# Kernel optimization log

Hardware: AMD Instinct MI355X
Metric: run time of the kernel (lower is better)

## Reference

```python
import jax, jax.numpy as jnp
import numpy as np

BS, GRID, LSTM_H, CNN_C, PROJ = 256, 49, 512, 2048, 512


def setup_inputs() -> dict:
    key = jax.random.key(0)
    ks = jax.random.split(key, 7)
    s = lambda fan_in: 1.0 / np.sqrt(fan_in)
    return {
        "lstm_hidden": jax.random.normal(ks[0], (BS, LSTM_H), jnp.float32),
        "cnn_feat": jax.random.normal(ks[1], (BS, GRID, CNN_C), jnp.float32),
        "W_lstm": jax.random.normal(ks[2], (PROJ, LSTM_H), jnp.float32) * s(LSTM_H),
        "b_lstm": jax.random.normal(ks[3], (PROJ,), jnp.float32) * s(LSTM_H),
        "W_cnn": jax.random.normal(ks[4], (PROJ, CNN_C), jnp.float32) * s(CNN_C),
        "b_cnn": jax.random.normal(ks[5], (PROJ,), jnp.float32) * s(CNN_C),
        "w_attn": jax.random.normal(ks[6], (1, PROJ), jnp.float32) * s(PROJ),
    }


def reference(lstm_hidden, cnn_feat, W_lstm, b_lstm, W_cnn, b_cnn, w_attn):
    # H computed once (original loop recomputes it per grid, identically)
    H = lstm_hidden @ W_lstm.T + b_lstm                       # (bs, P)
    V = jnp.einsum("bgc,pc->bgp", cnn_feat, W_cnn) + b_cnn    # (bs, G, P)
    z = jnp.tanh(H[:, None, :] + V) @ w_attn[0]               # (bs, G)
    bs, G = z.shape
    # Faithful to torch: cat over grids along dim 0 -> (G*bs,), then view(bs, G)
    z_scrambled = jnp.swapaxes(z, 0, 1).reshape(bs, G)
    return jax.nn.softmax(z_scrambled, axis=1)
```

## Files before the change

kernel.cpp:

```cpp
#include <hip/hip_runtime.h>
#include <math.h>

#define BSZ    256
#define GRID_N 49
#define LSTMH  512
#define CNN_C  2048
#define PROJ   512
#define KAUG   2560
#define M_TOT  12544
#define BK     64
#define KTILES (KAUG / BK)

#define MT     64
#define NT     128
#define NBLK   ((M_TOT / MT) * (PROJ / NT))

#define MT2    128
#define NT2    128
#define NBLK2  ((M_TOT / MT2) * (PROJ / NT2))

#define ACHUNKS (M_TOT * CNN_C / 8)
#define LCHUNKS (BSZ * LSTMH / 8)
#define ABLK    ((ACHUNKS + LCHUNKS) / 256)
#define WBLK    640
#define PBLK    (ABLK + WBLK)

typedef short bf16x8 __attribute__((ext_vector_type(8)));
typedef float f32x4  __attribute__((ext_vector_type(4)));

static __device__ __forceinline__ unsigned short bf16_rne(float f) {
    unsigned int u = __float_as_uint(f);
    u = u + 0x7FFFu + ((u >> 16) & 1u);
    return (unsigned short)(u >> 16);
}
static __device__ __forceinline__ uint4 pack8f(const float* f) {
    uint4 o;
    o.x = (unsigned int)bf16_rne(f[0]) | ((unsigned int)bf16_rne(f[1]) << 16);
    o.y = (unsigned int)bf16_rne(f[2]) | ((unsigned int)bf16_rne(f[3]) << 16);
    o.z = (unsigned int)bf16_rne(f[4]) | ((unsigned int)bf16_rne(f[5]) << 16);
    o.w = (unsigned int)bf16_rne(f[6]) | ((unsigned int)bf16_rne(f[7]) << 16);
    return o;
}
static __device__ __forceinline__ float tanh_fast(float x) {
    float e = __expf(2.f * x);
    return 1.f - 2.f / (e + 1.f);
}
static __device__ __forceinline__ void glds16(const void* g, void* l) {
    __builtin_amdgcn_global_load_lds(
        (const __attribute__((address_space(1))) unsigned int*)g,
        (__attribute__((address_space(3))) unsigned int*)l, 16, 0, 0);
}

__global__ __launch_bounds__(256) void prep_all(
    const float* __restrict__ cnn, const float* __restrict__ lstm,
    const float* __restrict__ Wc,  const float* __restrict__ Wl,
    unsigned short* __restrict__ wsW, unsigned short* __restrict__ wsA,
    unsigned short* __restrict__ wsL, float* __restrict__ out)
{
    const int bid = blockIdx.x, t = threadIdx.x;
    if (bid < 49) out[bid * 256 + t] = 0.f;
    float f[8];
    if (bid < ABLK) {
        const int c = bid * 256 + t;
        const float* src; unsigned short* dst;
        if (c < ACHUNKS) { src = cnn  + (size_t)c * 8; dst = wsA + (size_t)c * 8; }
        else { const int c2 = c - ACHUNKS; src = lstm + (size_t)c2 * 8; dst = wsL + (size_t)c2 * 8; }
        *(float4*)&f[0] = ((const float4*)src)[0];
        *(float4*)&f[4] = ((const float4*)src)[1];
        *(uint4*)dst = pack8f(f);
    } else {
        const int c  = (bid - ABLK) * 256 + t;
        const int p  = c / 320;
        const int kc = (c % 320) * 8;
        const float* src = (kc < CNN_C) ? (Wc + (size_t)p * CNN_C + kc)
                                        : (Wl + (size_t)p * LSTMH + (kc - CNN_C));
        *(float4*)&f[0] = ((const float4*)src)[0];
        *(float4*)&f[4] = ((const float4*)src)[1];
        *(uint4*)(wsW + (size_t)p * KAUG + kc) = pack8f(f);
    }
}

__global__ __launch_bounds__(256, 2) void gemm2(
    const unsigned short* __restrict__ wsW, const unsigned short* __restrict__ wsA,
    const unsigned short* __restrict__ wsL,
    const float* __restrict__ bl, const float* __restrict__ bc,
    const float* __restrict__ wat, float* __restrict__ out)
{
    __shared__ unsigned short Ab[2][MT2][BK];
    __shared__ unsigned short Bb[2][NT2][BK];

    const int t   = threadIdx.x;
    const int w   = t >> 6;
    const int l   = t & 63;
    const int q   = l >> 4;
    const int r16 = l & 15;
    const int wr  = w >> 1;
    const int wc  = w & 1;

    const int bid = (int)blockIdx.x;
    const int swz = (bid & 7) * (NBLK2 / 8) + (bid >> 3);
    const int m0  = (swz >> 2) * MT2;
    const int n0  = (swz & 3) * NT2;

    const int srow = l >> 3;
    const int cg   = (l & 7) ^ srow;

    auto stage = [&](int kt, int bufi) {
        const int k0 = kt * BK;
        #pragma unroll
        for (int jj = 0; jj < 4; ++jj) {
            const int rowb = w * 32 + jj * 8;
            const unsigned short* g = wsW + (size_t)(n0 + rowb + srow) * KAUG + k0 + cg * 8;
            glds16(g, &Bb[bufi][rowb][0]);
        }
        if (k0 < CNN_C) {
            #pragma unroll
            for (int jj = 0; jj < 4; ++jj) {
                const int rowa = w * 32 + jj * 8;
                const unsigned short* g = wsA + (size_t)(m0 + rowa + srow) * CNN_C + k0 + cg * 8;
                glds16(g, &Ab[bufi][rowa][0]);
            }
        } else {
            const int k0l = k0 - CNN_C;
            #pragma unroll
            for (int jj = 0; jj < 4; ++jj) {
                const int rowa = w * 32 + jj * 8;
                const int rg   = m0 + rowa + srow;
                const unsigned short* g = wsL + (size_t)(rg / 49) * LSTMH + k0l + cg * 8;
                glds16(g, &Ab[bufi][rowa][0]);
            }
        }
    };

    f32x4 acc[4][4];
    #pragma unroll
    for (int mt = 0; mt < 4; ++mt)
        #pragma unroll
        for (int nt = 0; nt < 4; ++nt)
            acc[mt][nt] = (f32x4){0.f, 0.f, 0.f, 0.f};

    stage(0, 0);
    asm volatile("s_waitcnt vmcnt(0)" ::: "memory");
    __builtin_amdgcn_s_barrier();

    int cur = 0;
    for (int kt = 0; kt < KTILES; ++kt) {
        if (kt + 1 < KTILES) stage(kt + 1, cur ^ 1);
        #pragma unroll
        for (int ks = 0; ks < 2; ++ks) {
            const int cp = ((ks * 4 + q) ^ (r16 & 7)) * 8;
            bf16x8 af[4], bfr[4];
            #pragma unroll
            for (int mt = 0; mt < 4; ++mt)
                af[mt] = *(const bf16x8*)&Ab[cur][wr * 64 + mt * 16 + r16][cp];
            #pragma unroll
            for (int nt = 0; nt < 4; ++nt)
                bfr[nt] = *(const bf16x8*)&Bb[cur][wc * 64 + nt * 16 + r16][cp];
            #pragma unroll
            for (int mt = 0; mt < 4; ++mt)
                #pragma unroll
                for (int nt = 0; nt < 4; ++nt)
                    acc[mt][nt] = __builtin_amdgcn_mfma_f32_16x16x32_bf16(
                        af[mt], bfr[nt], acc[mt][nt], 0, 0, 0);
        }
        asm volatile("s_waitcnt vmcnt(0)" ::: "memory");
        __builtin_amdgcn_s_barrier();
        cur ^= 1;
    }

    float* zpf = (float*)&Ab[0][0][0];
    float part[4][4];
    #pragma unroll
    for (int mt = 0; mt < 4; ++mt)
        #pragma unroll
        for (int rr = 0; rr < 4; ++rr) part[mt][rr] = 0.f;
    #pragma unroll
    for (int nt = 0; nt < 4; ++nt) {
        const int p = n0 + wc * 64 + nt * 16 + r16;
        const float bb = bl[p] + bc[p];
        const float wa = wat[p];
        #pragma unroll
        for (int mt = 0; mt < 4; ++mt)
            #pragma unroll
            for (int rr = 0; rr < 4; ++rr)
                part[mt][rr] += tanh_fast(acc[mt][nt][rr] + bb) * wa;
    }
    #pragma unroll
    for (int mt = 0; mt < 4; ++mt)
        #pragma unroll
        for (int rr = 0; rr < 4; ++rr) {
            float v = part[mt][rr];
            v += __shfl_xor(v, 1);
            v += __shfl_xor(v, 2);
            v += __shfl_xor(v, 4);
            v += __shfl_xor(v, 8);
            if (r16 == 0) zpf[wc * MT2 + wr * 64 + mt * 16 + q * 4 + rr] = v;
        }
    __syncthreads();
    if (t < MT2) {
        const float v = zpf[t] + zpf[MT2 + t];
        const int row = m0 + t;
        const int b2  = row / 49;
        const int g2  = row - b2 * 49;
        atomicAdd(&out[g2 * BSZ + b2], v);
    }
}

__global__ __launch_bounds__(256) void prep_w(const float* __restrict__ Wc,
                                              const float* __restrict__ Wl,
                                              unsigned short* __restrict__ wsW) {
    int c  = blockIdx.x * 256 + threadIdx.x;
    int p  = c / 320;
    int kc = (c % 320) * 8;
    const float* src = (kc < CNN_C) ? (Wc + (size_t)p * CNN_C + kc)
                                    : (Wl + (size_t)p * LSTMH + (kc - CNN_C));
    float f[8];
    *(float4*)&f[0] = ((const float4*)src)[0];
    *(float4*)&f[4] = ((const float4*)src)[1];
    *(uint4*)(wsW + (size_t)p * KAUG + kc) = pack8f(f);
}

template <bool WS>
__global__ __launch_bounds__(256, 4) void gemm_k(
    const float* __restrict__ lstm, const float* __restrict__ cnn,
    const float* __restrict__ Wc,   const float* __restrict__ Wl,
    const float* __restrict__ bl,   const float* __restrict__ bc,
    const float* __restrict__ wat,  const unsigned short* __restrict__ wsW,
    float* __restrict__ out)
{
    __shared__ unsigned short Ash[MT][BK];
    __shared__ unsigned short Bsh[NT][BK];
    __shared__ float zp[4][MT];

    const int t   = threadIdx.x;
    const int w   = t >> 6;
    const int l   = t & 63;
    const int q   = l >> 4;
    const int r16 = l & 15;

    const int bid = (int)blockIdx.x;
    const int swz = (bid & 7) * (NBLK / 8) + (bid >> 3);
    const int m0 = (swz >> 2) * MT;
    const int n0 = (swz & 3) * NT;

    const int ra  = t >> 2;
    const int ca0 = t & 3;
    const int sa  = ra & 7;
    const int grow = m0 + ra;
    const int ab   = grow / 49;
    const int ag   = grow - ab * 49;
    const float* cnnb  = cnn + ((size_t)ab * GRID_N + ag) * CNN_C;
    const float* lstmb = lstm + (size_t)ab * LSTMH;

    f32x4 acc[4][2];
    #pragma unroll
    for (int mt = 0; mt < 4; ++mt)
        #pragma unroll
        for (int nt = 0; nt < 2; ++nt)
            acc[mt][nt] = (f32x4){0.f, 0.f, 0.f, 0.f};

    float4 fa0, fa1, fa2, fa3;

    auto a_load = [&](int k0) {
        const float* s = (k0 < CNN_C) ? (cnnb + k0) : (lstmb + (k0 - CNN_C));
        const float4* p0 = (const float4*)(s + ca0 * 8);
        const float4* p1 = (const float4*)(s + (ca0 + 4) * 8);
        fa0 = p0[0]; fa1 = p0[1];
        fa2 = p1[0]; fa3 = p1[1];
    };
    auto a_write = [&]() {
        float f[8];
        *(float4*)&f[0] = fa0; *(float4*)&f[4] = fa1;
        *(uint4*)&Ash[ra][(ca0 ^ sa) * 8] = pack8f(f);
        *(float4*)&f[0] = fa2; *(float4*)&f[4] = fa3;
        *(uint4*)&Ash[ra][((ca0 + 4) ^ sa) * 8] = pack8f(f);
    };
    auto b_stage = [&](int k0) {
        if constexpr (WS) {
            const int rsub = l >> 3;
            const int cg   = (l & 7) ^ rsub;
            #pragma unroll
            for (int j = 0; j < 4; ++j) {
                const int rowb = w * 32 + j * 8;
                const unsigned short* g =
                    wsW + (size_t)(n0 + rowb + rsub) * KAUG + k0 + cg * 8;
                glds16(g, &Bsh[rowb][0]);
            }
        } else {
            const int rb = t >> 1;
            const int hb = t & 1;
            const float* s = (k0 < CNN_C) ? (Wc + (size_t)(n0 + rb) * CNN_C + k0)
                                          : (Wl + (size_t)(n0 + rb) * LSTMH + (k0 - CNN_C));
            const int sw = rb & 7;
            #pragma unroll
            for (int c = 0; c < 4; ++c) {
                const int cc = hb * 4 + c;
                float f[8];
                *(float4*)&f[0] = ((const float4*)(s + cc * 8))[0];
                *(float4*)&f[4] = ((const float4*)(s + cc * 8))[1];
                *(uint4*)&Bsh[rb][(cc ^ sw) * 8] = pack8f(f);
            }
        }
    };

    a_load(0);
    a_write();
    b_stage(0);

    for (int kt = 0; kt < KTILES; ++kt) {
        __syncthreads();
        const bool more = (kt + 1 < KTILES);
        if (more) a_load((kt + 1) * BK);
        #pragma unroll
        for (int ks = 0; ks < 2; ++ks) {
            const int cp = ((ks * 4 + q) ^ (r16 & 7)) * 8;
            bf16x8 af[4], bfr[2];
            #pragma unroll
            for (int mt = 0; mt < 4; ++mt)
                af[mt] = *(const bf16x8*)&Ash[mt * 16 + r16][cp];
            #pragma unroll
            for (int nt = 0; nt < 2; ++nt)
                bfr[nt] = *(const bf16x8*)&Bsh[w * 32 + nt * 16 + r16][cp];
            #pragma unroll
            for (int mt = 0; mt < 4; ++mt)
                #pragma unroll
                for (int nt = 0; nt < 2; ++nt)
                    acc[mt][nt] = __builtin_amdgcn_mfma_f32_16x16x32_bf16(
                        af[mt], bfr[nt], acc[mt][nt], 0, 0, 0);
        }
        __syncthreads();
        if (more) { a_write(); b_stage((kt + 1) * BK); }
    }

    float part[4][4];
    #pragma unroll
    for (int mt = 0; mt < 4; ++mt)
        #pragma unroll
        for (int rr = 0; rr < 4; ++rr) part[mt][rr] = 0.f;
    #pragma unroll
    for (int nt = 0; nt < 2; ++nt) {
        const int p = n0 + w * 32 + nt * 16 + r16;
        const float bb = bl[p] + bc[p];
        const float wa = wat[p];
        #pragma unroll
        for (int mt = 0; mt < 4; ++mt)
            #pragma unroll
            for (int rr = 0; rr < 4; ++rr)
                part[mt][rr] += tanh_fast(acc[mt][nt][rr] + bb) * wa;
    }
    #pragma unroll
    for (int mt = 0; mt < 4; ++mt)
        #pragma unroll
        for (int rr = 0; rr < 4; ++rr) {
            float v = part[mt][rr];
            v += __shfl_xor(v, 1);
            v += __shfl_xor(v, 2);
            v += __shfl_xor(v, 4);
            v += __shfl_xor(v, 8);
            if (r16 == 0) zp[w][mt * 16 + q * 4 + rr] = v;
        }
    __syncthreads();
    if (t < MT) {
        const float v = zp[0][t] + zp[1][t] + zp[2][t] + zp[3][t];
        const int row = m0 + t;
        const int b2  = row / 49;
        const int g2  = row - b2 * 49;
        atomicAdd(&out[g2 * BSZ + b2], v);
    }
}

__global__ __launch_bounds__(64) void softmax_rows(float* __restrict__ out)
{
    const int i = blockIdx.x;
    const int j = threadIdx.x;
    float x = (j < GRID_N) ? out[i * GRID_N + j] : -1e30f;
    float m = x;
    #pragma unroll
    for (int off = 32; off > 0; off >>= 1) m = fmaxf(m, __shfl_xor(m, off));
    float e = (j < GRID_N) ? __expf(x - m) : 0.f;
    float s = e;
    #pragma unroll
    for (int off = 32; off > 0; off >>= 1) s += __shfl_xor(s, off);
    if (j < GRID_N) out[i * GRID_N + j] = e / s;
}

extern "C" void kernel_launch(void* const* d_in, const int* in_sizes, int n_in,
                              void* d_out, int out_size, void* d_ws, size_t ws_size,
                              hipStream_t stream)
{
    const float* lstm = (const float*)d_in[0];
    const float* cnn  = (const float*)d_in[1];
    const float* Wl   = (const float*)d_in[2];
    const float* bl   = (const float*)d_in[3];
    const float* Wc   = (const float*)d_in[4];
    const float* bc   = (const float*)d_in[5];
    const float* wat  = (const float*)d_in[6];
    float* out = (float*)d_out;

    const size_t szW = (size_t)PROJ * KAUG * sizeof(unsigned short);
    const size_t szA = (size_t)M_TOT * CNN_C * sizeof(unsigned short);
    const size_t szL = (size_t)BSZ * LSTMH * sizeof(unsigned short);

    if (ws_size >= szW + szA + szL) {
        unsigned short* wsW = (unsigned short*)d_ws;
        unsigned short* wsA = wsW + (size_t)PROJ * KAUG;
        unsigned short* wsL = wsA + (size_t)M_TOT * CNN_C;
        prep_all<<<dim3(PBLK), dim3(256), 0, stream>>>(cnn, lstm, Wc, Wl, wsW, wsA, wsL, out);
        gemm2<<<dim3(NBLK2), dim3(256), 0, stream>>>(wsW, wsA, wsL, bl, bc, wat, out);
    } else if (ws_size >= szW) {
        hipMemsetAsync(out, 0, (size_t)out_size * sizeof(float), stream);
        unsigned short* wsW = (unsigned short*)d_ws;
        prep_w<<<dim3(WBLK), dim3(256), 0, stream>>>(Wc, Wl, wsW);
        gemm_k<true><<<dim3(NBLK), dim3(256), 0, stream>>>(lstm, cnn, Wc, Wl, bl, bc, wat, wsW, out);
    } else {
        hipMemsetAsync(out, 0, (size_t)out_size * sizeof(float), stream);
        gemm_k<false><<<dim3(NBLK), dim3(256), 0, stream>>>(lstm, cnn, Wc, Wl, bl, bc, wat, nullptr, out);
    }
    softmax_rows<<<dim3(BSZ), dim3(64), 0, stream>>>(out);
}
```

Measured before the change: 218.0 us.

## Fuse fp32-to-bf16 activation conversion into the GEMM mainloop, dropping the prep pass

Drops the separate pass that converted the full cnn_feat and lstm_hidden tensors to bf16 in workspace. The new GEMM loads fp32 activations straight from global memory into registers, packs them to bf16 and writes them into double-buffered LDS while the MFMAs on the current tile run. Only the weight matrix is still pre-converted, and the output zeroing moves into that small kernel. This removes a full-size write and re-read of the activation tensor. In exchange each A tile is read as fp32, twice the bytes, by every N-block, and register pressure in the mainloop goes up.

```diff
diff --git a/kernel.cpp b/kernel.cpp
--- a/kernel.cpp
+++ b/kernel.cpp
@@ -11,19 +11,15 @@
 #define BK     64
 #define KTILES (KAUG / BK)
 
+#define MT2    128
+#define NT2    128
+#define NBLK2  ((M_TOT / MT2) * (PROJ / NT2))
+
 #define MT     64
 #define NT     128
 #define NBLK   ((M_TOT / MT) * (PROJ / NT))
 
-#define MT2    128
-#define NT2    128
-#define NBLK2  ((M_TOT / MT2) * (PROJ / NT2))
-
-#define ACHUNKS (M_TOT * CNN_C / 8)
-#define LCHUNKS (BSZ * LSTMH / 8)
-#define ABLK    ((ACHUNKS + LCHUNKS) / 256)
-#define WBLK    640
-#define PBLK    (ABLK + WBLK)
+#define WBLK   640
 
 typedef short bf16x8 __attribute__((ext_vector_type(8)));
 typedef float f32x4  __attribute__((ext_vector_type(4)));
@@ -51,165 +47,13 @@
         (__attribute__((address_space(3))) unsigned int*)l, 16, 0, 0);
 }
 
-__global__ __launch_bounds__(256) void prep_all(
-    const float* __restrict__ cnn, const float* __restrict__ lstm,
-    const float* __restrict__ Wc,  const float* __restrict__ Wl,
-    unsigned short* __restrict__ wsW, unsigned short* __restrict__ wsA,
-    unsigned short* __restrict__ wsL, float* __restrict__ out)
-{
+__global__ __launch_bounds__(256) void prep_w(const float* __restrict__ Wc,
+                                              const float* __restrict__ Wl,
+                                              unsigned short* __restrict__ wsW,
+                                              float* __restrict__ out) {
     const int bid = blockIdx.x, t = threadIdx.x;
     if (bid < 49) out[bid * 256 + t] = 0.f;
-    float f[8];
-    if (bid < ABLK) {
-        const int c = bid * 256 + t;
-        const float* src; unsigned short* dst;
-        if (c < ACHUNKS) { src = cnn  + (size_t)c * 8; dst = wsA + (size_t)c * 8; }
-        else { const int c2 = c - ACHUNKS; src = lstm + (size_t)c2 * 8; dst = wsL + (size_t)c2 * 8; }
-        *(float4*)&f[0] = ((const float4*)src)[0];
-        *(float4*)&f[4] = ((const float4*)src)[1];
-        *(uint4*)dst = pack8f(f);
-    } else {
-        const int c  = (bid - ABLK) * 256 + t;
-        const int p  = c / 320;
-        const int kc = (c % 320) * 8;
-        const float* src = (kc < CNN_C) ? (Wc + (size_t)p * CNN_C + kc)
-                                        : (Wl + (size_t)p * LSTMH + (kc - CNN_C));
-        *(float4*)&f[0] = ((const float4*)src)[0];
-        *(float4*)&f[4] = ((const float4*)src)[1];
-        *(uint4*)(wsW + (size_t)p * KAUG + kc) = pack8f(f);
-    }
-}
-
-__global__ __launch_bounds__(256, 2) void gemm2(
-    const unsigned short* __restrict__ wsW, const unsigned short* __restrict__ wsA,
-    const unsigned short* __restrict__ wsL,
-    const float* __restrict__ bl, const float* __restrict__ bc,
-    const float* __restrict__ wat, float* __restrict__ out)
-{
-    __shared__ unsigned short Ab[2][MT2][BK];
-    __shared__ unsigned short Bb[2][NT2][BK];
-
-    const int t   = threadIdx.x;
-    const int w   = t >> 6;
-    const int l   = t & 63;
-    const int q   = l >> 4;
-    const int r16 = l & 15;
-    const int wr  = w >> 1;
-    const int wc  = w & 1;
-
-    const int bid = (int)blockIdx.x;
-    const int swz = (bid & 7) * (NBLK2 / 8) + (bid >> 3);
-    const int m0  = (swz >> 2) * MT2;
-    const int n0  = (swz & 3) * NT2;
-
-    const int srow = l >> 3;
-    const int cg   = (l & 7) ^ srow;
-
-    auto stage = [&](int kt, int bufi) {
-        const int k0 = kt * BK;
-        #pragma unroll
-        for (int jj = 0; jj < 4; ++jj) {
-            const int rowb = w * 32 + jj * 8;
-            const unsigned short* g = wsW + (size_t)(n0 + rowb + srow) * KAUG + k0 + cg * 8;
-            glds16(g, &Bb[bufi][rowb][0]);
-        }
-        if (k0 < CNN_C) {
-            #pragma unroll
-            for (int jj = 0; jj < 4; ++jj) {
-                const int rowa = w * 32 + jj * 8;
-                const unsigned short* g = wsA + (size_t)(m0 + rowa + srow) * CNN_C + k0 + cg * 8;
-                glds16(g, &Ab[bufi][rowa][0]);
-            }
-        } else {
-            const int k0l = k0 - CNN_C;
-            #pragma unroll
-            for (int jj = 0; jj < 4; ++jj) {
-                const int rowa = w * 32 + jj * 8;
-                const int rg   = m0 + rowa + srow;
-                const unsigned short* g = wsL + (size_t)(rg / 49) * LSTMH + k0l + cg * 8;
-                glds16(g, &Ab[bufi][rowa][0]);
-            }
-        }
-    };
-
-    f32x4 acc[4][4];
-    #pragma unroll
-    for (int mt = 0; mt < 4; ++mt)
-        #pragma unroll
-        for (int nt = 0; nt < 4; ++nt)
-            acc[mt][nt] = (f32x4){0.f, 0.f, 0.f, 0.f};
-
-    stage(0, 0);
-    asm volatile("s_waitcnt vmcnt(0)" ::: "memory");
-    __builtin_amdgcn_s_barrier();
-
-    int cur = 0;
-    for (int kt = 0; kt < KTILES; ++kt) {
-        if (kt + 1 < KTILES) stage(kt + 1, cur ^ 1);
-        #pragma unroll
-        for (int ks = 0; ks < 2; ++ks) {
-            const int cp = ((ks * 4 + q) ^ (r16 & 7)) * 8;
-            bf16x8 af[4], bfr[4];
-            #pragma unroll
-            for (int mt = 0; mt < 4; ++mt)
-                af[mt] = *(const bf16x8*)&Ab[cur][wr * 64 + mt * 16 + r16][cp];
-            #pragma unroll
-            for (int nt = 0; nt < 4; ++nt)
-                bfr[nt] = *(const bf16x8*)&Bb[cur][wc * 64 + nt * 16 + r16][cp];
-            #pragma unroll
-            for (int mt = 0; mt < 4; ++mt)
-                #pragma unroll
-                for (int nt = 0; nt < 4; ++nt)
-                    acc[mt][nt] = __builtin_amdgcn_mfma_f32_16x16x32_bf16(
-                        af[mt], bfr[nt], acc[mt][nt], 0, 0, 0);
-        }
-        asm volatile("s_waitcnt vmcnt(0)" ::: "memory");
-        __builtin_amdgcn_s_barrier();
-        cur ^= 1;
-    }
-
-    float* zpf = (float*)&Ab[0][0][0];
-    float part[4][4];
-    #pragma unroll
-    for (int mt = 0; mt < 4; ++mt)
-        #pragma unroll
-        for (int rr = 0; rr < 4; ++rr) part[mt][rr] = 0.f;
-    #pragma unroll
-    for (int nt = 0; nt < 4; ++nt) {
-        const int p = n0 + wc * 64 + nt * 16 + r16;
-        const float bb = bl[p] + bc[p];
-        const float wa = wat[p];
-        #pragma unroll
-        for (int mt = 0; mt < 4; ++mt)
-            #pragma unroll
-            for (int rr = 0; rr < 4; ++rr)
-                part[mt][rr] += tanh_fast(acc[mt][nt][rr] + bb) * wa;
-    }
-    #pragma unroll
-    for (int mt = 0; mt < 4; ++mt)
-        #pragma unroll
-        for (int rr = 0; rr < 4; ++rr) {
-            float v = part[mt][rr];
-            v += __shfl_xor(v, 1);
-            v += __shfl_xor(v, 2);
-            v += __shfl_xor(v, 4);
-            v += __shfl_xor(v, 8);
-            if (r16 == 0) zpf[wc * MT2 + wr * 64 + mt * 16 + q * 4 + rr] = v;
-        }
-    __syncthreads();
-    if (t < MT2) {
-        const float v = zpf[t] + zpf[MT2 + t];
-        const int row = m0 + t;
-        const int b2  = row / 49;
-        const int g2  = row - b2 * 49;
-        atomicAdd(&out[g2 * BSZ + b2], v);
-    }
-}
-
-__global__ __launch_bounds__(256) void prep_w(const float* __restrict__ Wc,
-                                              const float* __restrict__ Wl,
-                                              unsigned short* __restrict__ wsW) {
-    int c  = blockIdx.x * 256 + threadIdx.x;
+    int c  = bid * 256 + t;
     int p  = c / 320;
     int kc = (c % 320) * 8;
     const float* src = (kc < CNN_C) ? (Wc + (size_t)p * CNN_C + kc)
@@ -220,13 +64,150 @@
     *(uint4*)(wsW + (size_t)p * KAUG + kc) = pack8f(f);
 }
 
-template <bool WS>
+__global__ __launch_bounds__(256, 2) void gemm3(
+    const float* __restrict__ lstm, const float* __restrict__ cnn,
+    const unsigned short* __restrict__ wsW,
+    const float* __restrict__ bl, const float* __restrict__ bc,
+    const float* __restrict__ wat, float* __restrict__ out)
+{
+    __shared__ unsigned short Ab[2][MT2][BK];
+    __shared__ unsigned short Bb[2][NT2][BK];
+
+    const int t   = threadIdx.x;
+    const int w   = t >> 6;
+    const int l   = t & 63;
+    const int q   = l >> 4;
+    const int r16 = l & 15;
+    const int wr  = w >> 1;
+    const int wc  = w & 1;
+
+    const int bid = (int)blockIdx.x;
+    const int swz = (bid & 7) * (NBLK2 / 8) + (bid >> 3);
+    const int m0  = (swz >> 2) * MT2;
+    const int n0  = (swz & 3) * NT2;
+
+    const int ar  = t >> 1;
+    const int ac0 = (t & 1) * 4;
+    const int sw  = ar & 7;
+    const int grow = m0 + ar;
+    const int ab_  = grow / 49;
+    const int ag_  = grow - ab_ * 49;
+    const float* cnnb  = cnn + ((size_t)ab_ * GRID_N + ag_) * CNN_C;
+    const float* lstmb = lstm + (size_t)ab_ * LSTMH;
+
+    const int srow = l >> 3;
+    const int cg   = (l & 7) ^ srow;
+
+    float4 fa[8];
+    auto a_load = [&](int k0) {
+        const float* s = (((k0 < CNN_C) ? (cnnb + k0) : (lstmb + (k0 - CNN_C)))) + ac0 * 8;
+        #pragma unroll
+        for (int i = 0; i < 8; ++i) fa[i] = ((const float4*)s)[i];
+    };
+    auto a_write = [&](int bufi) {
+        #pragma unroll
+        for (int c = 0; c < 4; ++c) {
+            float f[8];
+            *(float4*)&f[0] = fa[2 * c];
+            *(float4*)&f[4] = fa[2 * c + 1];
+            *(uint4*)&Ab[bufi][ar][((ac0 + c) ^ sw) * 8] = pack8f(f);
+        }
+    };
+    auto b_stage = [&](int k0, int bufi) {
+        #pragma unroll
+        for (int jj = 0; jj < 4; ++jj) {
+            const int rowb = w * 32 + jj * 8;
+            const unsigned short* g = wsW + (size_t)(n0 + rowb + srow) * KAUG + k0 + cg * 8;
+            glds16(g, &Bb[bufi][rowb][0]);
+        }
+    };
+
+    f32x4 acc[4][4];
+    #pragma unroll
+    for (int mt = 0; mt < 4; ++mt)
+        #pragma unroll
+        for (int nt = 0; nt < 4; ++nt)
+            acc[mt][nt] = (f32x4){0.f, 0.f, 0.f, 0.f};
+
+    a_load(0);
+    a_write(0);
+    b_stage(0, 0);
+    asm volatile("s_waitcnt vmcnt(0) lgkmcnt(0)" ::: "memory");
+    __builtin_amdgcn_s_barrier();
+
+    int cur = 0;
+    for (int kt = 0; kt < KTILES; ++kt) {
+        const bool more = (kt + 1 < KTILES);
+        if (more) {
+            a_load((kt + 1) * BK);
+            b_stage((kt + 1) * BK, cur ^ 1);
+        }
+        #pragma unroll
+        for (int ks = 0; ks < 2; ++ks) {
+            const int cp = ((ks * 4 + q) ^ (r16 & 7)) * 8;
+            bf16x8 af[4], bfr[4];
+            #pragma unroll
+            for (int mt = 0; mt < 4; ++mt)
+                af[mt] = *(const bf16x8*)&Ab[cur][wr * 64 + mt * 16 + r16][cp];
+            #pragma unroll
+            for (int nt = 0; nt < 4; ++nt)
+                bfr[nt] = *(const bf16x8*)&Bb[cur][wc * 64 + nt * 16 + r16][cp];
+            #pragma unroll
+            for (int mt = 0; mt < 4; ++mt)
+                #pragma unroll
+                for (int nt = 0; nt < 4; ++nt)
+                    acc[mt][nt] = __builtin_amdgcn_mfma_f32_16x16x32_bf16(
+                        af[mt], bfr[nt], acc[mt][nt], 0, 0, 0);
+        }
+        if (more) a_write(cur ^ 1);
+        asm volatile("s_waitcnt vmcnt(0) lgkmcnt(0)" ::: "memory");
+        __builtin_amdgcn_s_barrier();
+        cur ^= 1;
+    }
+
+    float* zpf = (float*)&Ab[0][0][0];
+    float part[4][4];
+    #pragma unroll
+    for (int mt = 0; mt < 4; ++mt)
+        #pragma unroll
+        for (int rr = 0; rr < 4; ++rr) part[mt][rr] = 0.f;
+    #pragma unroll
+    for (int nt = 0; nt < 4; ++nt) {
+        const int p = n0 + wc * 64 + nt * 16 + r16;
+        const float bb = bl[p] + bc[p];
+        const float wa = wat[p];
+        #pragma unroll
+        for (int mt = 0; mt < 4; ++mt)
+            #pragma unroll
+            for (int rr = 0; rr < 4; ++rr)
+                part[mt][rr] += tanh_fast(acc[mt][nt][rr] + bb) * wa;
+    }
+    #pragma unroll
+    for (int mt = 0; mt < 4; ++mt)
+        #pragma unroll
+        for (int rr = 0; rr < 4; ++rr) {
+            float v = part[mt][rr];
+            v += __shfl_xor(v, 1);
+            v += __shfl_xor(v, 2);
+            v += __shfl_xor(v, 4);
+            v += __shfl_xor(v, 8);
+            if (r16 == 0) zpf[wc * MT2 + wr * 64 + mt * 16 + q * 4 + rr] = v;
+        }
+    __syncthreads();
+    if (t < MT2) {
+        const float v = zpf[t] + zpf[MT2 + t];
+        const int row = m0 + t;
+        const int b2  = row / 49;
+        const int g2  = row - b2 * 49;
+        atomicAdd(&out[g2 * BSZ + b2], v);
+    }
+}
+
 __global__ __launch_bounds__(256, 4) void gemm_k(
     const float* __restrict__ lstm, const float* __restrict__ cnn,
     const float* __restrict__ Wc,   const float* __restrict__ Wl,
     const float* __restrict__ bl,   const float* __restrict__ bc,
-    const float* __restrict__ wat,  const unsigned short* __restrict__ wsW,
-    float* __restrict__ out)
+    const float* __restrict__ wat,  float* __restrict__ out)
 {
     __shared__ unsigned short Ash[MT][BK];
     __shared__ unsigned short Bsh[NT][BK];
@@ -276,30 +257,18 @@
         *(uint4*)&Ash[ra][((ca0 + 4) ^ sa) * 8] = pack8f(f);
     };
     auto b_stage = [&](int k0) {
-        if constexpr (WS) {
-            const int rsub = l >> 3;
-            const int cg   = (l & 7) ^ rsub;
-            #pragma unroll
-            for (int j = 0; j < 4; ++j) {
-                const int rowb = w * 32 + j * 8;
-                const unsigned short* g =
-                    wsW + (size_t)(n0 + rowb + rsub) * KAUG + k0 + cg * 8;
-                glds16(g, &Bsh[rowb][0]);
-            }
-        } else {
-            const int rb = t >> 1;
-            const int hb = t & 1;
-            const float* s = (k0 < CNN_C) ? (Wc + (size_t)(n0 + rb) * CNN_C + k0)
-                                          : (Wl + (size_t)(n0 + rb) * LSTMH + (k0 - CNN_C));
-            const int sw = rb & 7;
-            #pragma unroll
-            for (int c = 0; c < 4; ++c) {
-                const int cc = hb * 4 + c;
-                float f[8];
-                *(float4*)&f[0] = ((const float4*)(s + cc * 8))[0];
-                *(float4*)&f[4] = ((const float4*)(s + cc * 8))[1];
-                *(uint4*)&Bsh[rb][(cc ^ sw) * 8] = pack8f(f);
-            }
+        const int rb = t >> 1;
+        const int hb = t & 1;
+        const float* s = (k0 < CNN_C) ? (Wc + (size_t)(n0 + rb) * CNN_C + k0)
+                                      : (Wl + (size_t)(n0 + rb) * LSTMH + (k0 - CNN_C));
+        const int sw = rb & 7;
+        #pragma unroll
+        for (int c = 0; c < 4; ++c) {
+            const int cc = hb * 4 + c;
+            float f[8];
+            *(float4*)&f[0] = ((const float4*)(s + cc * 8))[0];
+            *(float4*)&f[4] = ((const float4*)(s + cc * 8))[1];
+            *(uint4*)&Bsh[rb][(cc ^ sw) * 8] = pack8f(f);
         }
     };
 
@@ -398,23 +367,14 @@
     float* out = (float*)d_out;
 
     const size_t szW = (size_t)PROJ * KAUG * sizeof(unsigned short);
-    const size_t szA = (size_t)M_TOT * CNN_C * sizeof(unsigned short);
-    const size_t szL = (size_t)BSZ * LSTMH * sizeof(unsigned short);
-
-    if (ws_size >= szW + szA + szL) {
+
+    if (ws_size >= szW) {
         unsigned short* wsW = (unsigned short*)d_ws;
-        unsigned short* wsA = wsW + (size_t)PROJ * KAUG;
-        unsigned short* wsL = wsA + (size_t)M_TOT * CNN_C;
-        prep_all<<<dim3(PBLK), dim3(256), 0, stream>>>(cnn, lstm, Wc, Wl, wsW, wsA, wsL, out);
-        gemm2<<<dim3(NBLK2), dim3(256), 0, stream>>>(wsW, wsA, wsL, bl, bc, wat, out);
-    } else if (ws_size >= szW) {
-        hipMemsetAsync(out, 0, (size_t)out_size * sizeof(float), stream);
-        unsigned short* wsW = (unsigned short*)d_ws;
-        prep_w<<<dim3(WBLK), dim3(256), 0, stream>>>(Wc, Wl, wsW);
-        gemm_k<true><<<dim3(NBLK), dim3(256), 0, stream>>>(lstm, cnn, Wc, Wl, bl, bc, wat, wsW, out);
+        prep_w<<<dim3(WBLK), dim3(256), 0, stream>>>(Wc, Wl, wsW, out);
+        gemm3<<<dim3(NBLK2), dim3(256), 0, stream>>>(lstm, cnn, wsW, bl, bc, wat, out);
     } else {
         hipMemsetAsync(out, 0, (size_t)out_size * sizeof(float), stream);
-        gemm_k<false><<<dim3(NBLK), dim3(256), 0, stream>>>(lstm, cnn, Wc, Wl, bl, bc, wat, nullptr, out);
+        gemm_k<<<dim3(NBLK), dim3(256), 0, stream>>>(lstm, cnn, Wc, Wl, bl, bc, wat, out);
     }
     softmax_rows<<<dim3(BSZ), dim3(64), 0, stream>>>(out);
 }
```

Result: slower. 265.0 us (+21.6%).

## Split GEMM tile across eight waves with raised MFMA priority

Applied to the files above, without the earlier changes.

The main GEMM kernel now runs 512 threads (8 waves in a 2x4 grid) on the same 128x128 output tile, so each wave holds half the accumulators and the block asks for higher occupancy. It also raises wave priority around the MFMA section and waits on LDS counters before the barrier. The epilogue reduction now sums four column-wave partials. The intermediate workspace fallback path is removed. The risk is more barrier and synchronisation overhead and lower per-wave data reuse in exchange for more latency hiding.

```diff
diff --git a/kernel.cpp b/kernel.cpp
--- a/kernel.cpp
+++ b/kernel.cpp
@@ -11,13 +11,13 @@
 #define BK     64
 #define KTILES (KAUG / BK)
 
+#define MT2    128
+#define NT2    128
+#define NBLK2  ((M_TOT / MT2) * (PROJ / NT2))
+
 #define MT     64
 #define NT     128
 #define NBLK   ((M_TOT / MT) * (PROJ / NT))
-
-#define MT2    128
-#define NT2    128
-#define NBLK2  ((M_TOT / MT2) * (PROJ / NT2))
 
 #define ACHUNKS (M_TOT * CNN_C / 8)
 #define LCHUNKS (BSZ * LSTMH / 8)
@@ -80,7 +80,7 @@
     }
 }
 
-__global__ __launch_bounds__(256, 2) void gemm2(
+__global__ __launch_bounds__(512, 4) void gemm4(
     const unsigned short* __restrict__ wsW, const unsigned short* __restrict__ wsA,
     const unsigned short* __restrict__ wsL,
     const float* __restrict__ bl, const float* __restrict__ bc,
@@ -94,8 +94,8 @@
     const int l   = t & 63;
     const int q   = l >> 4;
     const int r16 = l & 15;
-    const int wr  = w >> 1;
-    const int wc  = w & 1;
+    const int wr  = w >> 2;
+    const int wc  = w & 3;
 
     const int bid = (int)blockIdx.x;
     const int swz = (bid & 7) * (NBLK2 / 8) + (bid >> 3);
@@ -108,23 +108,23 @@
     auto stage = [&](int kt, int bufi) {
         const int k0 = kt * BK;
         #pragma unroll
-        for (int jj = 0; jj < 4; ++jj) {
-            const int rowb = w * 32 + jj * 8;
+        for (int j = 0; j < 2; ++j) {
+            const int rowb = w * 16 + j * 8;
             const unsigned short* g = wsW + (size_t)(n0 + rowb + srow) * KAUG + k0 + cg * 8;
             glds16(g, &Bb[bufi][rowb][0]);
         }
         if (k0 < CNN_C) {
             #pragma unroll
-            for (int jj = 0; jj < 4; ++jj) {
-                const int rowa = w * 32 + jj * 8;
+            for (int j = 0; j < 2; ++j) {
+                const int rowa = w * 16 + j * 8;
                 const unsigned short* g = wsA + (size_t)(m0 + rowa + srow) * CNN_C + k0 + cg * 8;
                 glds16(g, &Ab[bufi][rowa][0]);
             }
         } else {
             const int k0l = k0 - CNN_C;
             #pragma unroll
-            for (int jj = 0; jj < 4; ++jj) {
-                const int rowa = w * 32 + jj * 8;
+            for (int j = 0; j < 2; ++j) {
+                const int rowa = w * 16 + j * 8;
                 const int rg   = m0 + rowa + srow;
                 const unsigned short* g = wsL + (size_t)(rg / 49) * LSTMH + k0l + cg * 8;
                 glds16(g, &Ab[bufi][rowa][0]);
@@ -132,11 +132,11 @@
         }
     };
 
-    f32x4 acc[4][4];
-    #pragma unroll
-    for (int mt = 0; mt < 4; ++mt)
-        #pragma unroll
-        for (int nt = 0; nt < 4; ++nt)
+    f32x4 acc[4][2];
+    #pragma unroll
+    for (int mt = 0; mt < 4; ++mt)
+        #pragma unroll
+        for (int nt = 0; nt < 2; ++nt)
             acc[mt][nt] = (f32x4){0.f, 0.f, 0.f, 0.f};
 
     stage(0, 0);
@@ -146,24 +146,26 @@
     int cur = 0;
     for (int kt = 0; kt < KTILES; ++kt) {
         if (kt + 1 < KTILES) stage(kt + 1, cur ^ 1);
+        __builtin_amdgcn_s_setprio(1);
         #pragma unroll
         for (int ks = 0; ks < 2; ++ks) {
             const int cp = ((ks * 4 + q) ^ (r16 & 7)) * 8;
-            bf16x8 af[4], bfr[4];
+            bf16x8 af[4], bfr[2];
             #pragma unroll
             for (int mt = 0; mt < 4; ++mt)
                 af[mt] = *(const bf16x8*)&Ab[cur][wr * 64 + mt * 16 + r16][cp];
             #pragma unroll
-            for (int nt = 0; nt < 4; ++nt)
-                bfr[nt] = *(const bf16x8*)&Bb[cur][wc * 64 + nt * 16 + r16][cp];
+            for (int nt = 0; nt < 2; ++nt)
+                bfr[nt] = *(const bf16x8*)&Bb[cur][wc * 32 + nt * 16 + r16][cp];
             #pragma unroll
             for (int mt = 0; mt < 4; ++mt)
                 #pragma unroll
-                for (int nt = 0; nt < 4; ++nt)
+                for (int nt = 0; nt < 2; ++nt)
                     acc[mt][nt] = __builtin_amdgcn_mfma_f32_16x16x32_bf16(
                         af[mt], bfr[nt], acc[mt][nt], 0, 0, 0);
         }
-        asm volatile("s_waitcnt vmcnt(0)" ::: "memory");
+        __builtin_amdgcn_s_setprio(0);
+        asm volatile("s_waitcnt vmcnt(0) lgkmcnt(0)" ::: "memory");
         __builtin_amdgcn_s_barrier();
         cur ^= 1;
     }
@@ -175,8 +177,8 @@
         #pragma unroll
         for (int rr = 0; rr < 4; ++rr) part[mt][rr] = 0.f;
     #pragma unroll
-    for (int nt = 0; nt < 4; ++nt) {
-        const int p = n0 + wc * 64 + nt * 16 + r16;
+    for (int nt = 0; nt < 2; ++nt) {
+        const int p = n0 + wc * 32 + nt * 16 + r16;
         const float bb = bl[p] + bc[p];
         const float wa = wat[p];
         #pragma unroll
@@ -198,7 +200,7 @@
         }
     __syncthreads();
     if (t < MT2) {
-        const float v = zpf[t] + zpf[MT2 + t];
+        const float v = zpf[t] + zpf[MT2 + t] + zpf[2 * MT2 + t] + zpf[3 * MT2 + t];
         const int row = m0 + t;
         const int b2  = row / 49;
         const int g2  = row - b2 * 49;
@@ -206,27 +208,11 @@
     }
 }
 
-__global__ __launch_bounds__(256) void prep_w(const float* __restrict__ Wc,
-                                              const float* __restrict__ Wl,
-                                              unsigned short* __restrict__ wsW) {
-    int c  = blockIdx.x * 256 + threadIdx.x;
-    int p  = c / 320;
-    int kc = (c % 320) * 8;
-    const float* src = (kc < CNN_C) ? (Wc + (size_t)p * CNN_C + kc)
-                                    : (Wl + (size_t)p * LSTMH + (kc - CNN_C));
-    float f[8];
-    *(float4*)&f[0] = ((const float4*)src)[0];
-    *(float4*)&f[4] = ((const float4*)src)[1];
-    *(uint4*)(wsW + (size_t)p * KAUG + kc) = pack8f(f);
-}
-
-template <bool WS>
 __global__ __launch_bounds__(256, 4) void gemm_k(
     const float* __restrict__ lstm, const float* __restrict__ cnn,
     const float* __restrict__ Wc,   const float* __restrict__ Wl,
     const float* __restrict__ bl,   const float* __restrict__ bc,
-    const float* __restrict__ wat,  const unsigned short* __restrict__ wsW,
-    float* __restrict__ out)
+    const float* __restrict__ wat,  float* __restrict__ out)
 {
     __shared__ unsigned short Ash[MT][BK];
     __shared__ unsigned short Bsh[NT][BK];
@@ -276,30 +262,18 @@
         *(uint4*)&Ash[ra][((ca0 + 4) ^ sa) * 8] = pack8f(f);
     };
     auto b_stage = [&](int k0) {
-        if constexpr (WS) {
-            const int rsub = l >> 3;
-            const int cg   = (l & 7) ^ rsub;
-            #pragma unroll
-            for (int j = 0; j < 4; ++j) {
-                const int rowb = w * 32 + j * 8;
-                const unsigned short* g =
-                    wsW + (size_t)(n0 + rowb + rsub) * KAUG + k0 + cg * 8;
-                glds16(g, &Bsh[rowb][0]);
-            }
-        } else {
-            const int rb = t >> 1;
-            const int hb = t & 1;
-            const float* s = (k0 < CNN_C) ? (Wc + (size_t)(n0 + rb) * CNN_C + k0)
-                                          : (Wl + (size_t)(n0 + rb) * LSTMH + (k0 - CNN_C));
-            const int sw = rb & 7;
-            #pragma unroll
-            for (int c = 0; c < 4; ++c) {
-                const int cc = hb * 4 + c;
-                float f[8];
-                *(float4*)&f[0] = ((const float4*)(s + cc * 8))[0];
-                *(float4*)&f[4] = ((const float4*)(s + cc * 8))[1];
-                *(uint4*)&Bsh[rb][(cc ^ sw) * 8] = pack8f(f);
-            }
+        const int rb = t >> 1;
+        const int hb = t & 1;
+        const float* s = (k0 < CNN_C) ? (Wc + (size_t)(n0 + rb) * CNN_C + k0)
+                                      : (Wl + (size_t)(n0 + rb) * LSTMH + (k0 - CNN_C));
+        const int sw = rb & 7;
+        #pragma unroll
+        for (int c = 0; c < 4; ++c) {
+            const int cc = hb * 4 + c;
+            float f[8];
+            *(float4*)&f[0] = ((const float4*)(s + cc * 8))[0];
+            *(float4*)&f[4] = ((const float4*)(s + cc * 8))[1];
+            *(uint4*)&Bsh[rb][(cc ^ sw) * 8] = pack8f(f);
         }
     };
 
@@ -406,15 +380,10 @@
         unsigned short* wsA = wsW + (size_t)PROJ * KAUG;
         unsigned short* wsL = wsA + (size_t)M_TOT * CNN_C;
         prep_all<<<dim3(PBLK), dim3(256), 0, stream>>>(cnn, lstm, Wc, Wl, wsW, wsA, wsL, out);
-        gemm2<<<dim3(NBLK2), dim3(256), 0, stream>>>(wsW, wsA, wsL, bl, bc, wat, out);
-    } else if (ws_size >= szW) {
-        hipMemsetAsync(out, 0, (size_t)out_size * sizeof(float), stream);
-        unsigned short* wsW = (unsigned short*)d_ws;
-        prep_w<<<dim3(WBLK), dim3(256), 0, stream>>>(Wc, Wl, wsW);
-        gemm_k<true><<<dim3(NBLK), dim3(256), 0, stream>>>(lstm, cnn, Wc, Wl, bl, bc, wat, wsW, out);
+        gemm4<<<dim3(NBLK2), dim3(512), 0, stream>>>(wsW, wsA, wsL, bl, bc, wat, out);
     } else {
         hipMemsetAsync(out, 0, (size_t)out_size * sizeof(float), stream);
-        gemm_k<false><<<dim3(NBLK), dim3(256), 0, stream>>>(lstm, cnn, Wc, Wl, bl, bc, wat, nullptr, out);
+        gemm_k<<<dim3(NBLK), dim3(256), 0, stream>>>(lstm, cnn, Wc, Wl, bl, bc, wat, out);
     }
     softmax_rows<<<dim3(BSZ), dim3(64), 0, stream>>>(out);
 }
```

New measurement: 217.6 us. Within noise of the previous version (-0.2%).
